# Performance work log

Hardware: AMD Instinct MI355X
Metric: run time of the kernel (lower is better)

## Reference

```python
import jax, jax.numpy as jnp
import numpy as np

N = 1_000_000   # pose-graph nodes
E = 2_000_000   # edges (odometry + loop closures)
M = N - 1
L1, L2, L3, L4 = 1.0, 0.1, 1.0, 0.1  # loss weights
EPS = 1e-8

# ---- quaternion / Lie-group helpers (pypose convention: [x,y,z,w]) ----

def qmul(q, r):
    qv, qw = q[..., :3], q[..., 3:]
    rv, rw = r[..., :3], r[..., 3:]
    w = qw * rw - jnp.sum(qv * rv, axis=-1, keepdims=True)
    v = qw * rv + rw * qv + jnp.cross(qv, rv)
    return jnp.concatenate([v, w], axis=-1)

def qconj(q):  # inverse of a unit quaternion
    return jnp.concatenate([-q[..., :3], q[..., 3:]], axis=-1)

def qrot(q, v):  # rotate vector v by unit quaternion q
    qv, qw = q[..., :3], q[..., 3:]
    t = 2.0 * jnp.cross(qv, v)
    return v + qw * t + jnp.cross(qv, t)

def so3_log(q):  # SO3 -> so3 rotation vector phi
    v, w = q[..., :3], q[..., 3]
    n = jnp.linalg.norm(v, axis=-1)
    theta = 2.0 * jnp.arctan2(n, w)
    big = n > EPS
    k = jnp.where(big, theta / jnp.where(big, n, 1.0), 2.0 / jnp.where(jnp.abs(w) > EPS, w, 1.0))
    return v * k[..., None]

def se3_log(t, q):  # SE3 -> se3 = [tau(3), phi(3)] (translation first, pypose order)
    phi = so3_log(q)
    theta2 = jnp.sum(phi * phi, axis=-1)
    theta = jnp.sqrt(theta2)
    small = theta < 1e-4
    ts = jnp.where(small, 1.0, theta)
    # V^{-1} coefficient: 1/theta^2 - (1+cos)/(2 theta sin); Taylor -> 1/12
    coef = jnp.where(small, 1.0 / 12.0,
                     1.0 / jnp.where(small, 1.0, theta2)
                     - (1.0 + jnp.cos(ts)) / (2.0 * ts * jnp.sin(ts)))
    pxt = jnp.cross(phi, t)
    tau = t - 0.5 * pxt + coef[..., None] * jnp.cross(phi, pxt)  # V^{-1} t without 3x3 mats
    return jnp.concatenate([tau, phi], axis=-1)

def _unit_quat(key, n):
    q = jax.random.normal(key, (n, 4), dtype=jnp.float32)
    return q / jnp.linalg.norm(q, axis=-1, keepdims=True)

def setup_inputs() -> dict:
    key = jax.random.key(0)
    k = jax.random.split(key, 9)
    nodes = jnp.concatenate([jax.random.normal(k[0], (N, 3), jnp.float32), _unit_quat(k[1], N)], axis=-1)
    vels = jax.random.normal(k[2], (N, 3), jnp.float32)
    edges = jax.random.randint(k[3], (E, 2), 0, N, dtype=jnp.int32)
    poses = jnp.concatenate([jax.random.normal(k[4], (E, 3), jnp.float32), _unit_quat(k[5], E)], axis=-1)
    imu_drots = _unit_quat(k[6], M)
    imu_dtrans = 0.1 * jax.random.normal(k[7], (M, 3), jnp.float32)
    imu_dvels = 0.1 * jax.random.normal(k[8], (M, 3), jnp.float32)
    dts = jnp.full((M, 1), 0.05, dtype=jnp.float32)
    return dict(edges=edges, nodes=nodes, vels=vels, poses=poses,
                imu_drots=imu_drots, imu_dtrans=imu_dtrans, imu_dvels=imu_dvels, dts=dts)

def reference(edges, nodes, vels, poses, imu_drots, imu_dtrans, imu_dvels, dts):
    t_n, q_n = nodes[:, :3], nodes[:, 3:]
    # --- pose-graph residual: (poses^-1 o node1^-1 o node2).Log() ---
    n1 = nodes[edges[:, 0]]
    n2 = nodes[edges[:, 1]]
    t1, q1 = n1[:, :3], n1[:, 3:]
    t2, q2 = n2[:, :3], n2[:, 3:]
    tp, qp = poses[:, :3], poses[:, 3:]
    qi1 = qconj(q1)
    ti1 = -qrot(qi1, t1)           # node1^-1
    qa = qmul(qi1, q2)
    ta = ti1 + qrot(qi1, t2)       # node1^-1 o node2
    qip = qconj(qp)
    tip = -qrot(qip, tp)           # poses^-1
    qe = qmul(qip, qa)
    te = tip + qrot(qip, ta)
    pgerr = se3_log(te, qe)                                   # [E, 6]
    # --- adjacent velocity residual ---
    adjvelerr = imu_dvels - (vels[1:] - vels[:-1])            # [M, 3]
    # --- IMU rotation residual: (drot^-1 o R1^-1 o R2).Log() ---
    qre = qmul(qconj(imu_drots), qmul(qconj(q_n[:-1]), q_n[1:]))
    imuroterr = so3_log(qre)                                  # [M, 3]
    # --- translation/velocity residual ---
    transvelerr = (t_n[1:] - t_n[:-1]) - (vels[:-1] * dts + imu_dtrans)  # [M, 3]
    return jnp.concatenate([L1 * pgerr.ravel(), L2 * adjvelerr.ravel(),
                            L3 * imuroterr.ravel(), L4 * transvelerr.ravel()], axis=0)
```

## Files before the change

kernel.cpp:

```cpp
#include <hip/hip_runtime.h>
#include <math.h>

#define EPS_Q 1e-8f

struct F3 { float x, y, z; };
struct Q4 { F3 v; float w; };

__device__ __forceinline__ F3 add3(F3 a, F3 b){ return {a.x+b.x, a.y+b.y, a.z+b.z}; }
__device__ __forceinline__ F3 sub3(F3 a, F3 b){ return {a.x-b.x, a.y-b.y, a.z-b.z}; }
__device__ __forceinline__ F3 scal3(float s, F3 a){ return {s*a.x, s*a.y, s*a.z}; }
__device__ __forceinline__ float dot3(F3 a, F3 b){ return a.x*b.x + a.y*b.y + a.z*b.z; }
__device__ __forceinline__ F3 cross3(F3 a, F3 b){
    return { a.y*b.z - a.z*b.y, a.z*b.x - a.x*b.z, a.x*b.y - a.y*b.x };
}
__device__ __forceinline__ Q4 qmul(Q4 q, Q4 r){
    Q4 o;
    o.w = q.w*r.w - dot3(q.v, r.v);
    o.v = add3(add3(scal3(q.w, r.v), scal3(r.w, q.v)), cross3(q.v, r.v));
    return o;
}
__device__ __forceinline__ Q4 qconj(Q4 q){ return { {-q.v.x, -q.v.y, -q.v.z}, q.w }; }
__device__ __forceinline__ F3 qrot(Q4 q, F3 v){
    F3 t = scal3(2.0f, cross3(q.v, v));
    return add3(add3(v, scal3(q.w, t)), cross3(q.v, t));
}
__device__ __forceinline__ F3 so3_log(Q4 q){
    float n = sqrtf(dot3(q.v, q.v));
    float theta = 2.0f * atan2f(n, q.w);
    float k;
    if (n > EPS_Q) k = theta / n;
    else           k = 2.0f / ((fabsf(q.w) > EPS_Q) ? q.w : 1.0f);
    return scal3(k, q.v);
}

__device__ __forceinline__ void edge_compute(F3 t1, Q4 q1, F3 t2, Q4 q2,
                                             F3 tp, Q4 qp, float* __restrict__ o)
{
    Q4 qi1 = qconj(q1);
    F3 ti1 = scal3(-1.0f, qrot(qi1, t1));
    Q4 qa  = qmul(qi1, q2);
    F3 ta  = add3(ti1, qrot(qi1, t2));

    Q4 qip = qconj(qp);
    F3 tip = scal3(-1.0f, qrot(qip, tp));
    Q4 qe  = qmul(qip, qa);
    F3 te  = add3(tip, qrot(qip, ta));

    F3 phi = so3_log(qe);
    float theta2 = dot3(phi, phi);
    float theta  = sqrtf(theta2);
    float coef;
    if (theta < 1e-4f) {
        coef = 1.0f / 12.0f;
    } else {
        coef = 1.0f / theta2 - (1.0f + cosf(theta)) / (2.0f * theta * sinf(theta));
    }
    F3 pxt = cross3(phi, te);
    F3 tau = add3(sub3(te, scal3(0.5f, pxt)), scal3(coef, cross3(phi, pxt)));

    o[0] = tau.x; o[1] = tau.y; o[2] = tau.z;
    o[3] = phi.x; o[4] = phi.y; o[5] = phi.z;
}

__global__ void pad_nodes_kernel(const float* __restrict__ nodes,
                                 float4* __restrict__ pn, int N)
{
    int i = blockIdx.x * blockDim.x + threadIdx.x;
    if (i >= N) return;
    const float* s = nodes + 7*(size_t)i;
    float4 a = { s[0], s[1], s[2], s[3] };
    float4 b = { s[4], s[5], s[6], 0.0f };
    pn[2*(size_t)i    ] = a;
    pn[2*(size_t)i + 1] = b;
}

__global__ void edge_kernel2(const int2*   __restrict__ edges,
                             const float4* __restrict__ pn,
                             const float*  __restrict__ poses,
                             float*        __restrict__ out,
                             int E, int half)
{
    int t = blockIdx.x * blockDim.x + threadIdx.x;
    if (t >= half) return;
    int e0 = t;
    int e1 = t + half;
    bool has1 = (e1 < E);
    int e1s = has1 ? e1 : e0;

    int2 ab0 = edges[e0];
    int2 ab1 = edges[e1s];

    float4 na0 = pn[2*(size_t)ab0.x], na1 = pn[2*(size_t)ab0.x + 1];
    float4 nb0 = pn[2*(size_t)ab0.y], nb1 = pn[2*(size_t)ab0.y + 1];
    float4 nc0 = pn[2*(size_t)ab1.x], nc1 = pn[2*(size_t)ab1.x + 1];
    float4 nd0 = pn[2*(size_t)ab1.y], nd1 = pn[2*(size_t)ab1.y + 1];

    const float* p0 = poses + 7*(size_t)e0;
    const float* p1 = poses + 7*(size_t)e1s;
    float pp0[7], pp1[7];
    #pragma unroll
    for (int k = 0; k < 7; ++k) pp0[k] = p0[k];
    #pragma unroll
    for (int k = 0; k < 7; ++k) pp1[k] = p1[k];

    {
        F3 t1 = {na0.x, na0.y, na0.z};  Q4 q1 = {{na0.w, na1.x, na1.y}, na1.z};
        F3 t2 = {nb0.x, nb0.y, nb0.z};  Q4 q2 = {{nb0.w, nb1.x, nb1.y}, nb1.z};
        F3 tp = {pp0[0], pp0[1], pp0[2]}; Q4 qp = {{pp0[3], pp0[4], pp0[5]}, pp0[6]};
        edge_compute(t1, q1, t2, q2, tp, qp, out + 6*(size_t)e0);
    }
    if (has1) {
        F3 t1 = {nc0.x, nc0.y, nc0.z};  Q4 q1 = {{nc0.w, nc1.x, nc1.y}, nc1.z};
        F3 t2 = {nd0.x, nd0.y, nd0.z};  Q4 q2 = {{nd0.w, nd1.x, nd1.y}, nd1.z};
        F3 tp = {pp1[0], pp1[1], pp1[2]}; Q4 qp = {{pp1[3], pp1[4], pp1[5]}, pp1[6]};
        edge_compute(t1, q1, t2, q2, tp, qp, out + 6*(size_t)e1);
    }
}

__global__ void node_kernel(const float4* __restrict__ pn,
                            const float*  __restrict__ vels,
                            const float4* __restrict__ imu_drots,
                            const float*  __restrict__ imu_dtrans,
                            const float*  __restrict__ imu_dvels,
                            const float*  __restrict__ dts,
                            float*        __restrict__ out,
                            int M,
                            size_t off_adjvel, size_t off_imurot, size_t off_transvel)
{
    int m = blockIdx.x * blockDim.x + threadIdx.x;
    if (m >= M) return;

    float4 n0a = pn[2*(size_t)m    ], n0b = pn[2*(size_t)m + 1];
    float4 n1a = pn[2*(size_t)m + 2], n1b = pn[2*(size_t)m + 3];
    F3 t0 = {n0a.x, n0a.y, n0a.z};  Q4 q0 = {{n0a.w, n0b.x, n0b.y}, n0b.z};
    F3 t1 = {n1a.x, n1a.y, n1a.z};  Q4 q1 = {{n1a.w, n1b.x, n1b.y}, n1b.z};

    F3 v0 = {vels[3*(size_t)m],     vels[3*(size_t)m + 1], vels[3*(size_t)m + 2]};
    F3 v1 = {vels[3*(size_t)m + 3], vels[3*(size_t)m + 4], vels[3*(size_t)m + 5]};

    F3 dvm = {imu_dvels[3*(size_t)m], imu_dvels[3*(size_t)m + 1], imu_dvels[3*(size_t)m + 2]};
    F3 adjv = sub3(dvm, sub3(v1, v0));
    out[off_adjvel + 3*(size_t)m    ] = 0.1f * adjv.x;
    out[off_adjvel + 3*(size_t)m + 1] = 0.1f * adjv.y;
    out[off_adjvel + 3*(size_t)m + 2] = 0.1f * adjv.z;

    float4 drv = imu_drots[m];
    Q4 dr = {{drv.x, drv.y, drv.z}, drv.w};
    Q4 qre = qmul(qconj(dr), qmul(qconj(q0), q1));
    F3 rot = so3_log(qre);
    out[off_imurot + 3*(size_t)m    ] = rot.x;
    out[off_imurot + 3*(size_t)m + 1] = rot.y;
    out[off_imurot + 3*(size_t)m + 2] = rot.z;

    float dt = dts[m];
    F3 dtr = {imu_dtrans[3*(size_t)m], imu_dtrans[3*(size_t)m + 1], imu_dtrans[3*(size_t)m + 2]};
    F3 tv = sub3(sub3(t1, t0), add3(scal3(dt, v0), dtr));
    out[off_transvel + 3*(size_t)m    ] = 0.1f * tv.x;
    out[off_transvel + 3*(size_t)m + 1] = 0.1f * tv.y;
    out[off_transvel + 3*(size_t)m + 2] = 0.1f * tv.z;
}

__global__ void edge_kernel(const int*   __restrict__ edges,
                            const float* __restrict__ nodes,
                            const float* __restrict__ poses,
                            float*       __restrict__ out,
                            int E)
{
    int e = blockIdx.x * blockDim.x + threadIdx.x;
    if (e >= E) return;
    int i = edges[2*(size_t)e];
    int j = edges[2*(size_t)e + 1];
    const float* n1 = nodes + 7*(size_t)i;
    const float* n2 = nodes + 7*(size_t)j;
    const float* p  = poses + 7*(size_t)e;
    F3 t1 = {n1[0], n1[1], n1[2]};  Q4 q1 = {{n1[3], n1[4], n1[5]}, n1[6]};
    F3 t2 = {n2[0], n2[1], n2[2]};  Q4 q2 = {{n2[3], n2[4], n2[5]}, n2[6]};
    F3 tp = {p[0],  p[1],  p[2]};   Q4 qp = {{p[3],  p[4],  p[5]},  p[6]};
    edge_compute(t1, q1, t2, q2, tp, qp, out + 6*(size_t)e);
}

__global__ void node_kernel_raw(const float* __restrict__ nodes,
                                const float* __restrict__ vels,
                                const float* __restrict__ imu_drots,
                                const float* __restrict__ imu_dtrans,
                                const float* __restrict__ imu_dvels,
                                const float* __restrict__ dts,
                                float*       __restrict__ out,
                                int M,
                                size_t off_adjvel, size_t off_imurot, size_t off_transvel)
{
    int m = blockIdx.x * blockDim.x + threadIdx.x;
    if (m >= M) return;
    const float* n0 = nodes + 7*(size_t)m;
    const float* n1 = nodes + 7*(size_t)(m+1);
    F3 t0 = {n0[0], n0[1], n0[2]};  Q4 q0 = {{n0[3], n0[4], n0[5]}, n0[6]};
    F3 t1 = {n1[0], n1[1], n1[2]};  Q4 q1 = {{n1[3], n1[4], n1[5]}, n1[6]};
    F3 v0 = {vels[3*(size_t)m],     vels[3*(size_t)m + 1], vels[3*(size_t)m + 2]};
    F3 v1 = {vels[3*(size_t)m + 3], vels[3*(size_t)m + 4], vels[3*(size_t)m + 5]};
    F3 dvm = {imu_dvels[3*(size_t)m], imu_dvels[3*(size_t)m + 1], imu_dvels[3*(size_t)m + 2]};
    F3 adjv = sub3(dvm, sub3(v1, v0));
    out[off_adjvel + 3*(size_t)m    ] = 0.1f * adjv.x;
    out[off_adjvel + 3*(size_t)m + 1] = 0.1f * adjv.y;
    out[off_adjvel + 3*(size_t)m + 2] = 0.1f * adjv.z;
    Q4 dr = {{imu_drots[4*(size_t)m], imu_drots[4*(size_t)m + 1], imu_drots[4*(size_t)m + 2]},
              imu_drots[4*(size_t)m + 3]};
    Q4 qre = qmul(qconj(dr), qmul(qconj(q0), q1));
    F3 rot = so3_log(qre);
    out[off_imurot + 3*(size_t)m    ] = rot.x;
    out[off_imurot + 3*(size_t)m + 1] = rot.y;
    out[off_imurot + 3*(size_t)m + 2] = rot.z;
    float dt = dts[m];
    F3 dtr = {imu_dtrans[3*(size_t)m], imu_dtrans[3*(size_t)m + 1], imu_dtrans[3*(size_t)m + 2]};
    F3 tv = sub3(sub3(t1, t0), add3(scal3(dt, v0), dtr));
    out[off_transvel + 3*(size_t)m    ] = 0.1f * tv.x;
    out[off_transvel + 3*(size_t)m + 1] = 0.1f * tv.y;
    out[off_transvel + 3*(size_t)m + 2] = 0.1f * tv.z;
}

extern "C" void kernel_launch(void* const* d_in, const int* in_sizes, int n_in,
                              void* d_out, int out_size, void* d_ws, size_t ws_size,
                              hipStream_t stream) {
    const int*   edges      = (const int*)  d_in[0];
    const float* nodes      = (const float*)d_in[1];
    const float* vels       = (const float*)d_in[2];
    const float* poses      = (const float*)d_in[3];
    const float* imu_drots  = (const float*)d_in[4];
    const float* imu_dtrans = (const float*)d_in[5];
    const float* imu_dvels  = (const float*)d_in[6];
    const float* dts        = (const float*)d_in[7];
    float* out = (float*)d_out;

    const int E = in_sizes[0] / 2;
    const int N = in_sizes[1] / 7;
    const int M = in_sizes[7];

    const size_t off_adjvel   = 6*(size_t)E;
    const size_t off_imurot   = off_adjvel + 3*(size_t)M;
    const size_t off_transvel = off_imurot + 3*(size_t)M;

    const int BLK = 256;
    const size_t need = 2 * (size_t)N * sizeof(float4);

    if (ws_size >= need) {
        float4* pn = (float4*)d_ws;
        pad_nodes_kernel<<<(N + BLK - 1) / BLK, BLK, 0, stream>>>(nodes, pn, N);
        const int half = (E + 1) / 2;
        edge_kernel2<<<(half + BLK - 1) / BLK, BLK, 0, stream>>>(
            (const int2*)edges, pn, poses, out, E, half);
        node_kernel<<<(M + BLK - 1) / BLK, BLK, 0, stream>>>(
            pn, vels, (const float4*)imu_drots, imu_dtrans, imu_dvels, dts, out, M,
            off_adjvel, off_imurot, off_transvel);
    } else {
        edge_kernel<<<(E + BLK - 1) / BLK, BLK, 0, stream>>>(edges, nodes, poses, out, E);
        node_kernel_raw<<<(M + BLK - 1) / BLK, BLK, 0, stream>>>(nodes, vels, imu_drots, imu_dtrans,
                                                                 imu_dvels, dts, out, M,
                                                                 off_adjvel, off_imurot, off_transvel);
    }
}
```

Measured before the change: 275.8 us.

## Fuse node padding with node residuals and process four edges per thread with vector loads

```diff
diff --git a/kernel.cpp b/kernel.cpp
--- a/kernel.cpp
+++ b/kernel.cpp
@@ -2,6 +2,9 @@
 #include <math.h>
 
 #define EPS_Q 1e-8f
+
+typedef float vfloat4 __attribute__((ext_vector_type(4)));
+typedef int   vint4   __attribute__((ext_vector_type(4)));
 
 struct F3 { float x, y, z; };
 struct Q4 { F3 v; float w; };
@@ -53,7 +56,9 @@
     if (theta < 1e-4f) {
         coef = 1.0f / 12.0f;
     } else {
-        coef = 1.0f / theta2 - (1.0f + cosf(theta)) / (2.0f * theta * sinf(theta));
+        float s, c;
+        sincosf(theta, &s, &c);
+        coef = 1.0f / theta2 - (1.0f + c) / (2.0f * theta * s);
     }
     F3 pxt = cross3(phi, te);
     F3 tau = add3(sub3(te, scal3(0.5f, pxt)), scal3(coef, cross3(phi, pxt)));
@@ -62,78 +67,77 @@
     o[3] = phi.x; o[4] = phi.y; o[5] = phi.z;
 }
 
-__global__ void pad_nodes_kernel(const float* __restrict__ nodes,
-                                 float4* __restrict__ pn, int N)
-{
-    int i = blockIdx.x * blockDim.x + threadIdx.x;
-    if (i >= N) return;
-    const float* s = nodes + 7*(size_t)i;
-    float4 a = { s[0], s[1], s[2], s[3] };
-    float4 b = { s[4], s[5], s[6], 0.0f };
-    pn[2*(size_t)i    ] = a;
-    pn[2*(size_t)i + 1] = b;
-}
-
-__global__ void edge_kernel2(const int2*   __restrict__ edges,
-                             const float4* __restrict__ pn,
-                             const float*  __restrict__ poses,
-                             float*        __restrict__ out,
-                             int E, int half)
+__global__ __launch_bounds__(256, 3)
+void edge_kernel4(const int*   __restrict__ edges_raw,
+                  const float4* __restrict__ pn,
+                  const float*  __restrict__ poses_raw,
+                  float4*       __restrict__ out4,
+                  int ngroups)
 {
     int t = blockIdx.x * blockDim.x + threadIdx.x;
-    if (t >= half) return;
-    int e0 = t;
-    int e1 = t + half;
-    bool has1 = (e1 < E);
-    int e1s = has1 ? e1 : e0;
-
-    int2 ab0 = edges[e0];
-    int2 ab1 = edges[e1s];
-
-    float4 na0 = pn[2*(size_t)ab0.x], na1 = pn[2*(size_t)ab0.x + 1];
-    float4 nb0 = pn[2*(size_t)ab0.y], nb1 = pn[2*(size_t)ab0.y + 1];
-    float4 nc0 = pn[2*(size_t)ab1.x], nc1 = pn[2*(size_t)ab1.x + 1];
-    float4 nd0 = pn[2*(size_t)ab1.y], nd1 = pn[2*(size_t)ab1.y + 1];
-
-    const float* p0 = poses + 7*(size_t)e0;
-    const float* p1 = poses + 7*(size_t)e1s;
-    float pp0[7], pp1[7];
-    #pragma unroll
-    for (int k = 0; k < 7; ++k) pp0[k] = p0[k];
-    #pragma unroll
-    for (int k = 0; k < 7; ++k) pp1[k] = p1[k];
-
-    {
-        F3 t1 = {na0.x, na0.y, na0.z};  Q4 q1 = {{na0.w, na1.x, na1.y}, na1.z};
-        F3 t2 = {nb0.x, nb0.y, nb0.z};  Q4 q2 = {{nb0.w, nb1.x, nb1.y}, nb1.z};
-        F3 tp = {pp0[0], pp0[1], pp0[2]}; Q4 qp = {{pp0[3], pp0[4], pp0[5]}, pp0[6]};
-        edge_compute(t1, q1, t2, q2, tp, qp, out + 6*(size_t)e0);
-    }
-    if (has1) {
-        F3 t1 = {nc0.x, nc0.y, nc0.z};  Q4 q1 = {{nc0.w, nc1.x, nc1.y}, nc1.z};
-        F3 t2 = {nd0.x, nd0.y, nd0.z};  Q4 q2 = {{nd0.w, nd1.x, nd1.y}, nd1.z};
-        F3 tp = {pp1[0], pp1[1], pp1[2]}; Q4 qp = {{pp1[3], pp1[4], pp1[5]}, pp1[6]};
-        edge_compute(t1, q1, t2, q2, tp, qp, out + 6*(size_t)e1);
-    }
-}
-
-__global__ void node_kernel(const float4* __restrict__ pn,
-                            const float*  __restrict__ vels,
-                            const float4* __restrict__ imu_drots,
-                            const float*  __restrict__ imu_dtrans,
-                            const float*  __restrict__ imu_dvels,
-                            const float*  __restrict__ dts,
-                            float*        __restrict__ out,
-                            int M,
-                            size_t off_adjvel, size_t off_imurot, size_t off_transvel)
+    if (t >= ngroups) return;
+
+    const vint4* edges4 = (const vint4*)edges_raw;
+    vint4 eA = __builtin_nontemporal_load(edges4 + 2*(size_t)t);
+    vint4 eB = __builtin_nontemporal_load(edges4 + 2*(size_t)t + 1);
+    int idx[8] = {eA.x, eA.y, eA.z, eA.w, eB.x, eB.y, eB.z, eB.w};
+
+    float4 na[8], nb[8];
+    #pragma unroll
+    for (int r = 0; r < 8; ++r) {
+        na[r] = pn[2*(size_t)idx[r]];
+        nb[r] = pn[2*(size_t)idx[r] + 1];
+    }
+
+    const vfloat4* poses4 = (const vfloat4*)poses_raw;
+    vfloat4 P[7];
+    #pragma unroll
+    for (int k = 0; k < 7; ++k)
+        P[k] = __builtin_nontemporal_load(poses4 + 7*(size_t)t + k);
+    const float* pp = (const float*)P;
+
+    float ores[24];
+    #pragma unroll
+    for (int r = 0; r < 4; ++r) {
+        F3 t1 = {na[2*r].x, na[2*r].y, na[2*r].z};
+        Q4 q1 = {{na[2*r].w, nb[2*r].x, nb[2*r].y}, nb[2*r].z};
+        F3 t2 = {na[2*r+1].x, na[2*r+1].y, na[2*r+1].z};
+        Q4 q2 = {{na[2*r+1].w, nb[2*r+1].x, nb[2*r+1].y}, nb[2*r+1].z};
+        F3 tp = {pp[7*r+0], pp[7*r+1], pp[7*r+2]};
+        Q4 qp = {{pp[7*r+3], pp[7*r+4], pp[7*r+5]}, pp[7*r+6]};
+        edge_compute(t1, q1, t2, q2, tp, qp, ores + 6*r);
+    }
+
+    float4* o4 = out4 + 6*(size_t)t;
+    const float4* ov = (const float4*)ores;
+    #pragma unroll
+    for (int k = 0; k < 6; ++k) o4[k] = ov[k];
+}
+
+__global__ void node_pad_kernel(const float*  __restrict__ nodes,
+                                float4*       __restrict__ pn,
+                                const float*  __restrict__ vels,
+                                const float4* __restrict__ imu_drots,
+                                const float*  __restrict__ imu_dtrans,
+                                const float*  __restrict__ imu_dvels,
+                                const float*  __restrict__ dts,
+                                float*        __restrict__ out,
+                                int M, int N,
+                                size_t off_adjvel, size_t off_imurot, size_t off_transvel)
 {
     int m = blockIdx.x * blockDim.x + threadIdx.x;
+    if (m >= N) return;
+
+    const float* s0 = nodes + 7*(size_t)m;
+    float a0=s0[0], a1=s0[1], a2=s0[2], a3=s0[3], a4=s0[4], a5=s0[5], a6=s0[6];
+    pn[2*(size_t)m    ] = {a0, a1, a2, a3};
+    pn[2*(size_t)m + 1] = {a4, a5, a6, 0.0f};
+
     if (m >= M) return;
 
-    float4 n0a = pn[2*(size_t)m    ], n0b = pn[2*(size_t)m + 1];
-    float4 n1a = pn[2*(size_t)m + 2], n1b = pn[2*(size_t)m + 3];
-    F3 t0 = {n0a.x, n0a.y, n0a.z};  Q4 q0 = {{n0a.w, n0b.x, n0b.y}, n0b.z};
-    F3 t1 = {n1a.x, n1a.y, n1a.z};  Q4 q1 = {{n1a.w, n1b.x, n1b.y}, n1b.z};
+    const float* s1 = nodes + 7*(size_t)(m+1);
+    F3 t0 = {a0, a1, a2};  Q4 q0 = {{a3, a4, a5}, a6};
+    F3 t1 = {s1[0], s1[1], s1[2]};  Q4 q1 = {{s1[3], s1[4], s1[5]}, s1[6]};
 
     F3 v0 = {vels[3*(size_t)m],     vels[3*(size_t)m + 1], vels[3*(size_t)m + 2]};
     F3 v1 = {vels[3*(size_t)m + 3], vels[3*(size_t)m + 4], vels[3*(size_t)m + 5]};
@@ -158,6 +162,53 @@
     out[off_transvel + 3*(size_t)m    ] = 0.1f * tv.x;
     out[off_transvel + 3*(size_t)m + 1] = 0.1f * tv.y;
     out[off_transvel + 3*(size_t)m + 2] = 0.1f * tv.z;
+}
+
+__global__ void edge_kernel2(const int2*   __restrict__ edges,
+                             const float4* __restrict__ pn,
+                             const float*  __restrict__ poses,
+                             float*        __restrict__ out,
+                             int E, int half)
+{
+    int t = blockIdx.x * blockDim.x + threadIdx.x;
+    if (t >= half) return;
+    int e0 = t;
+    int e1 = t + half;
+    bool has1 = (e1 < E);
+    int e1s = has1 ? e1 : e0;
+    int2 ab0 = edges[e0];
+    int2 ab1 = edges[e1s];
+    float4 na0 = pn[2*(size_t)ab0.x], na1 = pn[2*(size_t)ab0.x + 1];
+    float4 nb0 = pn[2*(size_t)ab0.y], nb1 = pn[2*(size_t)ab0.y + 1];
+    float4 nc0 = pn[2*(size_t)ab1.x], nc1 = pn[2*(size_t)ab1.x + 1];
+    float4 nd0 = pn[2*(size_t)ab1.y], nd1 = pn[2*(size_t)ab1.y + 1];
+    const float* p0 = poses + 7*(size_t)e0;
+    const float* p1 = poses + 7*(size_t)e1s;
+    float pp0[7], pp1[7];
+    #pragma unroll
+    for (int k = 0; k < 7; ++k) pp0[k] = p0[k];
+    #pragma unroll
+    for (int k = 0; k < 7; ++k) pp1[k] = p1[k];
+    {
+        F3 t1 = {na0.x, na0.y, na0.z};  Q4 q1 = {{na0.w, na1.x, na1.y}, na1.z};
+        F3 t2 = {nb0.x, nb0.y, nb0.z};  Q4 q2 = {{nb0.w, nb1.x, nb1.y}, nb1.z};
+        F3 tp = {pp0[0], pp0[1], pp0[2]}; Q4 qp = {{pp0[3], pp0[4], pp0[5]}, pp0[6]};
+        float o[6];
+        edge_compute(t1, q1, t2, q2, tp, qp, o);
+        float* dst = out + 6*(size_t)e0;
+        #pragma unroll
+        for (int k = 0; k < 6; ++k) dst[k] = o[k];
+    }
+    if (has1) {
+        F3 t1 = {nc0.x, nc0.y, nc0.z};  Q4 q1 = {{nc0.w, nc1.x, nc1.y}, nc1.z};
+        F3 t2 = {nd0.x, nd0.y, nd0.z};  Q4 q2 = {{nd0.w, nd1.x, nd1.y}, nd1.z};
+        F3 tp = {pp1[0], pp1[1], pp1[2]}; Q4 qp = {{pp1[3], pp1[4], pp1[5]}, pp1[6]};
+        float o[6];
+        edge_compute(t1, q1, t2, q2, tp, qp, o);
+        float* dst = out + 6*(size_t)e1;
+        #pragma unroll
+        for (int k = 0; k < 6; ++k) dst[k] = o[k];
+    }
 }
 
 __global__ void edge_kernel(const int*   __restrict__ edges,
@@ -176,7 +227,11 @@
     F3 t1 = {n1[0], n1[1], n1[2]};  Q4 q1 = {{n1[3], n1[4], n1[5]}, n1[6]};
     F3 t2 = {n2[0], n2[1], n2[2]};  Q4 q2 = {{n2[3], n2[4], n2[5]}, n2[6]};
     F3 tp = {p[0],  p[1],  p[2]};   Q4 qp = {{p[3],  p[4],  p[5]},  p[6]};
-    edge_compute(t1, q1, t2, q2, tp, qp, out + 6*(size_t)e);
+    float o[6];
+    edge_compute(t1, q1, t2, q2, tp, qp, o);
+    float* dst = out + 6*(size_t)e;
+    #pragma unroll
+    for (int k = 0; k < 6; ++k) dst[k] = o[k];
 }
 
 __global__ void node_kernel_raw(const float* __restrict__ nodes,
@@ -243,13 +298,18 @@
 
     if (ws_size >= need) {
         float4* pn = (float4*)d_ws;
-        pad_nodes_kernel<<<(N + BLK - 1) / BLK, BLK, 0, stream>>>(nodes, pn, N);
-        const int half = (E + 1) / 2;
-        edge_kernel2<<<(half + BLK - 1) / BLK, BLK, 0, stream>>>(
-            (const int2*)edges, pn, poses, out, E, half);
-        node_kernel<<<(M + BLK - 1) / BLK, BLK, 0, stream>>>(
-            pn, vels, (const float4*)imu_drots, imu_dtrans, imu_dvels, dts, out, M,
-            off_adjvel, off_imurot, off_transvel);
+        node_pad_kernel<<<(N + BLK - 1) / BLK, BLK, 0, stream>>>(
+            nodes, pn, vels, (const float4*)imu_drots, imu_dtrans, imu_dvels, dts,
+            out, M, N, off_adjvel, off_imurot, off_transvel);
+        if ((E & 3) == 0) {
+            const int ngroups = E / 4;
+            edge_kernel4<<<(ngroups + BLK - 1) / BLK, BLK, 0, stream>>>(
+                edges, pn, poses, (float4*)out, ngroups);
+        } else {
+            const int half = (E + 1) / 2;
+            edge_kernel2<<<(half + BLK - 1) / BLK, BLK, 0, stream>>>(
+                (const int2*)edges, pn, poses, out, E, half);
+        }
     } else {
         edge_kernel<<<(E + BLK - 1) / BLK, BLK, 0, stream>>>(edges, nodes, poses, out, E);
         node_kernel_raw<<<(M + BLK - 1) / BLK, BLK, 0, stream>>>(nodes, vels, imu_drots, imu_dtrans,
```

After: 298.6 us. 8.3% more time.
